# Kernel optimization log

Hardware: AMD Instinct MI355X
Metric: run time of the kernel (lower is better)

## Reference

```python
import jax, jax.numpy as jnp
import numpy as np

NUM_FRAMES = 10000
NR = 2_000_000


def _vec2skew(v):
    # Faithful to ExtrinsicsLearner.vec2skew: columns are s0,s1,s2 (stack along dim=2).
    zero = jnp.zeros_like(v[:, 0])
    s0 = jnp.stack([zero, -v[:, 2], v[:, 1]], axis=1)   # (nr, 3)
    s1 = jnp.stack([v[:, 2], zero, -v[:, 0]], axis=1)
    s2 = jnp.stack([-v[:, 1], v[:, 0], zero], axis=1)
    return jnp.stack([s0, s1, s2], axis=2)              # (nr, 3, 3)


def _exp_so3(r):
    # Rodrigues formula, matching Exp(): eps added to norm, not norm^2 clamped.
    skew = _vec2skew(r)                                  # (nr, 3, 3)
    n = jnp.linalg.norm(r, axis=1) + 1e-15               # (nr,)
    eye = jnp.eye(3, dtype=r.dtype)
    a = (jnp.sin(n) / n)[:, None, None]
    b = ((1.0 - jnp.cos(n)) / (n * n))[:, None, None]
    return eye[None] + a * skew + b * (skew @ skew)


def setup_inputs() -> dict:
    key = jax.random.key(0)
    k1, k2, k3, k4, k5 = jax.random.split(key, 5)
    # Learned per-frame pose corrections (small, as after a few optim steps)
    r = jax.random.normal(k1, (NUM_FRAMES, 3), dtype=jnp.float32) * 0.05
    t = jax.random.normal(k2, (NUM_FRAMES, 3), dtype=jnp.float32) * 0.05
    # Initial extrinsics: valid rigid transforms (R0 | t0; 0 0 0 1)
    r0 = jax.random.normal(k3, (NUM_FRAMES, 3), dtype=jnp.float32) * 0.5
    R0 = _exp_so3(r0)                                    # (N, 3, 3)
    t0 = jax.random.normal(k4, (NUM_FRAMES, 3, 1), dtype=jnp.float32)
    top = jnp.concatenate([R0, t0], axis=2)              # (N, 3, 4)
    bottom = jnp.broadcast_to(
        jnp.array([[0.0, 0.0, 0.0, 1.0]], dtype=jnp.float32), (NUM_FRAMES, 1, 4))
    initial_extrinsics = jnp.concatenate([top, bottom], axis=1)  # (N, 4, 4)
    cam_id = jax.random.randint(k5, (NR,), 0, NUM_FRAMES, dtype=jnp.int64)
    return {"r": r, "t": t, "initial_extrinsics": initial_extrinsics,
            "cam_id": cam_id}


def reference(r, t, initial_extrinsics, cam_id):
    rg = r[cam_id]                                       # (nr, 3) gather
    tg = t[cam_id]                                       # (nr, 3)
    R = _exp_so3(rg)                                     # (nr, 3, 3)
    c2w34 = jnp.concatenate([R, tg[:, :, None]], axis=2)  # (nr, 3, 4)
    bottom = jnp.broadcast_to(
        jnp.array([[0.0, 0.0, 0.0, 1.0]], dtype=c2w34.dtype), (rg.shape[0], 1, 4))
    c2w = jnp.concatenate([c2w34, bottom], axis=1)       # (nr, 4, 4)
    extrinsics = jnp.linalg.inv(c2w)                     # batched 4x4 inverse
    return initial_extrinsics[cam_id] @ extrinsics       # (nr, 4, 4)
```

## Files before the change

### kernel.cpp

```cpp
#include <hip/hip_runtime.h>

typedef float f4 __attribute__((ext_vector_type(4)));

__global__ __launch_bounds__(256) void fused_row_kernel(
        const float* __restrict__ r,
        const float* __restrict__ t,
        const float* __restrict__ e0,
        const int* __restrict__ cid,
        f4* __restrict__ out, int n4) {
    const int tid = blockIdx.x * blockDim.x + threadIdx.x;
    if (tid >= n4) return;
    const int ray = tid >> 2;
    const int c   = tid & 3;
    const int f   = cid[ray];

    const float rx = r[3 * f + 0], ry = r[3 * f + 1], rz = r[3 * f + 2];
    const float tx = t[3 * f + 0], ty = t[3 * f + 1], tz = t[3 * f + 2];

    const float s = rx * rx + ry * ry + rz * rz;
    const float n = sqrtf(s) + 1e-15f;
    const float sn = sinf(n), cn = cosf(n);
    const float A = sn / n;
    const float B = (1.0f - cn) / (n * n);

    const float R00 = 1.0f + B * (rx * rx - s);
    const float R01 =  A * rz + B * (rx * ry);
    const float R02 = -A * ry + B * (rx * rz);
    const float R10 = -A * rz + B * (rx * ry);
    const float R11 = 1.0f + B * (ry * ry - s);
    const float R12 =  A * rx + B * (ry * rz);
    const float R20 =  A * ry + B * (rx * rz);
    const float R21 = -A * rx + B * (ry * rz);
    const float R22 = 1.0f + B * (rz * rz - s);

    const float T00 = R00, T01 = R10, T02 = R20;
    const float T10 = R01, T11 = R11, T12 = R21;
    const float T20 = R02, T21 = R12, T22 = R22;
    const float u0 = -(T00 * tx + T01 * ty + T02 * tz);
    const float u1 = -(T10 * tx + T11 * ty + T12 * tz);
    const float u2 = -(T20 * tx + T21 * ty + T22 * tz);

    const f4 e = *reinterpret_cast<const f4*>(e0 + 16 * f + 4 * c);

    f4 m;
    m.x = e.x * T00 + e.y * T10 + e.z * T20;
    m.y = e.x * T01 + e.y * T11 + e.z * T21;
    m.z = e.x * T02 + e.y * T12 + e.z * T22;
    m.w = e.x * u0 + e.y * u1 + e.z * u2 + e.w;

    __builtin_nontemporal_store(m, out + tid);
}

extern "C" void kernel_launch(void* const* d_in, const int* in_sizes, int n_in,
                              void* d_out, int out_size, void* d_ws, size_t ws_size,
                              hipStream_t stream) {
    const float* r  = (const float*)d_in[0];
    const float* t  = (const float*)d_in[1];
    const float* e0 = (const float*)d_in[2];
    const int*  cid = (const int*)d_in[3];
    float* out = (float*)d_out;

    const int nr = in_sizes[3];
    const int n4 = nr * 4;
    const int threads = 256;
    const int blocks = (n4 + threads - 1) / threads;
    fused_row_kernel<<<blocks, threads, 0, stream>>>(
        r, t, e0, cid, (f4*)out, n4);
}
```

Before: 176.1 us.

## Precompute per-frame 3x4 transform table, then gather rows per ray

Splits the work into two kernels. The first computes the composed initial-extrinsics times inverse-pose matrix once per frame (10k frames) into a workspace table. The second gathers table rows per ray and writes the constant bottom row directly. This removes the per-ray sin/cos and matrix math, which was repeated about 200 times per frame, at the cost of an extra launch and a dependent table read. It also drops the nontemporal store, and falls back to a fused per-ray kernel when the workspace is too small.

New measurement: 158.4 us. 10.1% less time.

```diff
diff --git a/kernel.cpp b/kernel.cpp
--- a/kernel.cpp
+++ b/kernel.cpp
@@ -2,17 +2,12 @@
 
 typedef float f4 __attribute__((ext_vector_type(4)));
 
-__global__ __launch_bounds__(256) void fused_row_kernel(
-        const float* __restrict__ r,
-        const float* __restrict__ t,
-        const float* __restrict__ e0,
-        const int* __restrict__ cid,
-        f4* __restrict__ out, int n4) {
-    const int tid = blockIdx.x * blockDim.x + threadIdx.x;
-    if (tid >= n4) return;
-    const int ray = tid >> 2;
-    const int c   = tid & 3;
-    const int f   = cid[ray];
+__global__ void build_table_kernel(const float* __restrict__ r,
+                                   const float* __restrict__ t,
+                                   const float* __restrict__ e0,
+                                   float* __restrict__ M, int nf) {
+    int f = blockIdx.x * blockDim.x + threadIdx.x;
+    if (f >= nf) return;
 
     const float rx = r[3 * f + 0], ry = r[3 * f + 1], rz = r[3 * f + 2];
     const float tx = t[3 * f + 0], ty = t[3 * f + 1], tz = t[3 * f + 2];
@@ -40,15 +35,81 @@
     const float u1 = -(T10 * tx + T11 * ty + T12 * tz);
     const float u2 = -(T20 * tx + T21 * ty + T22 * tz);
 
-    const f4 e = *reinterpret_cast<const f4*>(e0 + 16 * f + 4 * c);
+    const float* E = e0 + 16 * f;
+    f4* Mo = reinterpret_cast<f4*>(M + 12 * f);
+    #pragma unroll
+    for (int i = 0; i < 3; ++i) {
+        const float a0 = E[4 * i + 0], a1 = E[4 * i + 1];
+        const float a2 = E[4 * i + 2], a3 = E[4 * i + 3];
+        f4 m;
+        m.x = a0 * T00 + a1 * T10 + a2 * T20;
+        m.y = a0 * T01 + a1 * T11 + a2 * T21;
+        m.z = a0 * T02 + a1 * T12 + a2 * T22;
+        m.w = a0 * u0 + a1 * u1 + a2 * u2 + a3;
+        Mo[i] = m;
+    }
+}
 
-    f4 m;
-    m.x = e.x * T00 + e.y * T10 + e.z * T20;
-    m.y = e.x * T01 + e.y * T11 + e.z * T21;
-    m.z = e.x * T02 + e.y * T12 + e.z * T22;
-    m.w = e.x * u0 + e.y * u1 + e.z * u2 + e.w;
+__global__ __launch_bounds__(256) void gather_kernel(
+        const int* __restrict__ cid,
+        const f4* __restrict__ M,
+        f4* __restrict__ out, int n4) {
+    const int tid = blockIdx.x * blockDim.x + threadIdx.x;
+    if (tid >= n4) return;
+    const int ray = tid >> 2;
+    const int c   = tid & 3;
+    f4 m = {0.0f, 0.0f, 0.0f, 1.0f};
+    if (c < 3) {
+        const int cam = cid[ray];
+        m = M[cam * 3 + c];
+    }
+    out[tid] = m;
+}
 
-    __builtin_nontemporal_store(m, out + tid);
+__global__ void fused_kernel(const float* __restrict__ r,
+                             const float* __restrict__ t,
+                             const float* __restrict__ e0,
+                             const int* __restrict__ cid,
+                             f4* __restrict__ out, int nr) {
+    int ray = blockIdx.x * blockDim.x + threadIdx.x;
+    if (ray >= nr) return;
+    const int f = cid[ray];
+
+    const float rx = r[3 * f + 0], ry = r[3 * f + 1], rz = r[3 * f + 2];
+    const float tx = t[3 * f + 0], ty = t[3 * f + 1], tz = t[3 * f + 2];
+    const float s = rx * rx + ry * ry + rz * rz;
+    const float n = sqrtf(s) + 1e-15f;
+    const float sn = sinf(n), cn = cosf(n);
+    const float A = sn / n;
+    const float B = (1.0f - cn) / (n * n);
+    const float R00 = 1.0f + B * (rx * rx - s);
+    const float R01 =  A * rz + B * (rx * ry);
+    const float R02 = -A * ry + B * (rx * rz);
+    const float R10 = -A * rz + B * (rx * ry);
+    const float R11 = 1.0f + B * (ry * ry - s);
+    const float R12 =  A * rx + B * (ry * rz);
+    const float R20 =  A * ry + B * (rx * rz);
+    const float R21 = -A * rx + B * (ry * rz);
+    const float R22 = 1.0f + B * (rz * rz - s);
+    const float T00 = R00, T01 = R10, T02 = R20;
+    const float T10 = R01, T11 = R11, T12 = R21;
+    const float T20 = R02, T21 = R12, T22 = R22;
+    const float u0 = -(T00 * tx + T01 * ty + T02 * tz);
+    const float u1 = -(T10 * tx + T11 * ty + T12 * tz);
+    const float u2 = -(T20 * tx + T21 * ty + T22 * tz);
+
+    const float* E = e0 + 16 * f;
+    #pragma unroll
+    for (int i = 0; i < 4; ++i) {
+        const float a0 = E[4 * i + 0], a1 = E[4 * i + 1];
+        const float a2 = E[4 * i + 2], a3 = E[4 * i + 3];
+        f4 m;
+        m.x = a0 * T00 + a1 * T10 + a2 * T20;
+        m.y = a0 * T01 + a1 * T11 + a2 * T21;
+        m.z = a0 * T02 + a1 * T12 + a2 * T22;
+        m.w = a0 * u0 + a1 * u1 + a2 * u2 + a3;
+        out[(size_t)ray * 4 + i] = m;
+    }
 }
 
 extern "C" void kernel_launch(void* const* d_in, const int* in_sizes, int n_in,
@@ -60,10 +121,28 @@
     const int*  cid = (const int*)d_in[3];
     float* out = (float*)d_out;
 
+    const int nf = in_sizes[0] / 3;
     const int nr = in_sizes[3];
-    const int n4 = nr * 4;
-    const int threads = 256;
-    const int blocks = (n4 + threads - 1) / threads;
-    fused_row_kernel<<<blocks, threads, 0, stream>>>(
-        r, t, e0, cid, (f4*)out, n4);
+    const size_t table_bytes = (size_t)nf * 12 * sizeof(float);
+
+    if (ws_size >= table_bytes) {
+        float* M = (float*)d_ws;
+        {
+            int threads = 256;
+            int blocks = (nf + threads - 1) / threads;
+            build_table_kernel<<<blocks, threads, 0, stream>>>(r, t, e0, M, nf);
+        }
+        {
+            const int n4 = nr * 4;
+            int threads = 256;
+            int blocks = (n4 + threads - 1) / threads;
+            gather_kernel<<<blocks, threads, 0, stream>>>(
+                cid, (const f4*)M, (f4*)out, n4);
+        }
+    } else {
+        int threads = 256;
+        int blocks = (nr + threads - 1) / threads;
+        fused_kernel<<<blocks, threads, 0, stream>>>(
+            r, t, e0, cid, (f4*)out, nr);
+    }
 }
```
